# Optimization experiments

Measured on AMD Instinct MI355X. Metric: run time of the kernel, lower is better.

## Reference

```python
import jax, jax.numpy as jnp
import numpy as np

MAX_ANTS = 16  # padded max draws per (batch, neuron); ragged draws masked with -1
BS, N_IN, N_OUT = 32, 4096, 4096


def setup_inputs() -> dict:
    key = jax.random.key(0)
    k1, k2 = jax.random.split(key)
    # integer ant counts per (batch, input neuron), in [0, MAX_ANTS)
    x = jax.random.randint(k1, (BS, N_IN), 0, MAX_ANTS, dtype=jnp.int32)
    # positive weights (original init is uniform 1/n_outputs; random positive is general)
    weights = jax.random.uniform(k2, (N_IN, N_OUT), dtype=jnp.float32, minval=0.01, maxval=1.0)
    return {"x": x, "weights": weights}


def reference(x, weights):
    """Vectorized equivalent of ACOLayer.forward.

    Original: for each batch b and input neuron i with count c = x[b, i] > 0,
    draw c iid categorical samples from row-normalized weights[i].
    Here: inverse-CDF sampling, padded to MAX_ANTS draws, invalid slots = -1.
    Returns int32 [bs, n_in, MAX_ANTS].
    """
    probs = weights / weights.sum(axis=1, keepdims=True)   # normalize()
    cdf = jnp.cumsum(probs, axis=1)                        # [n_in, n_out]
    bs, n_in = x.shape
    n_out = weights.shape[1]
    u = jax.random.uniform(jax.random.key(42), (bs, n_in, MAX_ANTS), dtype=weights.dtype)
    # group draws by input neuron so each row's CDF is searched once
    u_rows = u.transpose(1, 0, 2).reshape(n_in, bs * MAX_ANTS)  # [n_in, bs*MAX]
    idx = jax.vmap(jnp.searchsorted)(cdf, u_rows)               # inverse-CDF draw
    idx = jnp.minimum(idx, n_out - 1).astype(jnp.int32)
    idx = idx.reshape(n_in, bs, MAX_ANTS).transpose(1, 0, 2)    # [bs, n_in, MAX]
    valid = jnp.arange(MAX_ANTS, dtype=x.dtype)[None, None, :] < x[:, :, None]
    return jnp.where(valid, idx, -1)
```

## Files before the change

### kernel.cpp

```cpp
#include <hip/hip_runtime.h>
#include <stdint.h>


#define N_IN    4096
#define N_OUT   4096
#define BS      32
#define MAX_A   16
#define THREADS 256
#define HALF    1048576u

__device__ __forceinline__ int padi(int j) { return j + (j >> 5); }

__device__ __forceinline__ uint32_t rotl32(uint32_t x, uint32_t r) {
    return (x << r) | (x >> (32u - r));
}

__device__ __forceinline__ void threefry2x32_42(uint32_t x0, uint32_t x1,
                                                uint32_t& o0, uint32_t& o1) {
    const uint32_t k0 = 0u, k1 = 42u;
    const uint32_t k2 = k0 ^ k1 ^ 0x1BD11BDAu;
    x0 += k0; x1 += k1;
#define TF_R(r) { x0 += x1; x1 = rotl32(x1, (r)); x1 ^= x0; }
    TF_R(13) TF_R(15) TF_R(26) TF_R(6)
    x0 += k1; x1 += k2 + 1u;
    TF_R(17) TF_R(29) TF_R(16) TF_R(24)
    x0 += k2; x1 += k0 + 2u;
    TF_R(13) TF_R(15) TF_R(26) TF_R(6)
    x0 += k0; x1 += k1 + 3u;
    TF_R(17) TF_R(29) TF_R(16) TF_R(24)
    x0 += k1; x1 += k2 + 4u;
    TF_R(13) TF_R(15) TF_R(26) TF_R(6)
    x0 += k2; x1 += k0 + 5u;
#undef TF_R
    o0 = x0; o1 = x1;
}

__device__ __forceinline__ float bits_to_uniform(uint32_t b) {
    uint32_t f = (b >> 9) | 0x3f800000u;
    float r;
    __builtin_memcpy(&r, &f, 4);
    return r - 1.0f;
}

__device__ __forceinline__ int tree4(float t,
    float T1, float T2, float T3, float T4, float T5, float T6, float T7,
    float T8, float T9, float T10, float T11, float T12, float T13,
    float T14, float T15) {
    const bool c1 = (T8 < t);
    const float m2 = c1 ? T12 : T4;
    const bool c2 = (m2 < t);
    const float ma = c2 ? T6  : T2;
    const float mb = c2 ? T14 : T10;
    const float m3 = c1 ? mb : ma;
    const bool c3 = (m3 < t);
    const float a1 = c3 ? T3  : T1;
    const float a2 = c3 ? T7  : T5;
    const float a3 = c3 ? T11 : T9;
    const float a4 = c3 ? T15 : T13;
    const float b1 = c2 ? a2 : a1;
    const float b2 = c2 ? a4 : a3;
    const float m4 = c1 ? b2 : b1;
    const bool c4 = (m4 < t);
    return (c1 ? 8 : 0) | (c2 ? 4 : 0) | (c3 ? 2 : 0) | (c4 ? 1 : 0);
}

__global__ __launch_bounds__(THREADS)
void aco_sample_kernel(const int* __restrict__ x,
                       const float* __restrict__ w,
                       int* __restrict__ out) {
    __shared__ float cdf[N_OUT + (N_OUT >> 5)];
    __shared__ float wsum[4];
    __shared__ int   xc[BS];

    const int row  = blockIdx.x;
    const int t    = threadIdx.x;
    const int lane = t & 63;
    const int wid  = t >> 6;

    const float4* wrow = (const float4*)(w + (size_t)row * N_OUT);
    float4 v0 = wrow[t * 4 + 0];
    float4 v1 = wrow[t * 4 + 1];
    float4 v2 = wrow[t * 4 + 2];
    float4 v3 = wrow[t * 4 + 3];

    if (t < BS) xc[t] = x[t * N_IN + row];

    const int bb = t >> 4;
    const int aa = t & 15;
    const uint32_t j0 = (uint32_t)(bb * (N_IN * MAX_A) + row * MAX_A + aa);
    const uint32_t j1 = j0 + HALF;
    uint32_t o0, o1, p0, p1;
    threefry2x32_42(0u, j0, o0, o1);
    threefry2x32_42(0u, j1, p0, p1);
    const float u0 = bits_to_uniform(o0 ^ o1);
    const float u1 = bits_to_uniform(p0 ^ p1);

    float loc[16];
    {
        float s = 0.f;
        s += v0.x; loc[0]  = s;  s += v0.y; loc[1]  = s;
        s += v0.z; loc[2]  = s;  s += v0.w; loc[3]  = s;
        s += v1.x; loc[4]  = s;  s += v1.y; loc[5]  = s;
        s += v1.z; loc[6]  = s;  s += v1.w; loc[7]  = s;
        s += v2.x; loc[8]  = s;  s += v2.y; loc[9]  = s;
        s += v2.z; loc[10] = s;  s += v2.w; loc[11] = s;
        s += v3.x; loc[12] = s;  s += v3.y; loc[13] = s;
        s += v3.z; loc[14] = s;  s += v3.w; loc[15] = s;
    }
    const float my_total = loc[15];

    float incl = my_total;
    #pragma unroll
    for (int d = 1; d < 64; d <<= 1) {
        float n = __shfl_up(incl, d, 64);
        if (lane >= d) incl += n;
    }
    if (lane == 63) wsum[wid] = incl;
    __syncthreads();

    const float4 ws = *(const float4*)wsum;
    const float total = ws.x + ws.y + ws.z + ws.w;
    float wprefix = 0.f;
    if (wid > 0) wprefix += ws.x;
    if (wid > 1) wprefix += ws.y;
    if (wid > 2) wprefix += ws.z;
    const float chunk_prefix = wprefix + incl - my_total;

    {
        const int base = t * 16;
        #pragma unroll
        for (int m = 0; m < 16; ++m)
            cdf[padi(base + m)] = chunk_prefix + loc[m];
    }
    __syncthreads();

    const float T1  = cdf[padi( 1 << 8)];
    const float T2  = cdf[padi( 2 << 8)];
    const float T3  = cdf[padi( 3 << 8)];
    const float T4  = cdf[padi( 4 << 8)];
    const float T5  = cdf[padi( 5 << 8)];
    const float T6  = cdf[padi( 6 << 8)];
    const float T7  = cdf[padi( 7 << 8)];
    const float T8  = cdf[padi( 8 << 8)];
    const float T9  = cdf[padi( 9 << 8)];
    const float T10 = cdf[padi(10 << 8)];
    const float T11 = cdf[padi(11 << 8)];
    const float T12 = cdf[padi(12 << 8)];
    const float T13 = cdf[padi(13 << 8)];
    const float T14 = cdf[padi(14 << 8)];
    const float T15 = cdf[padi(15 << 8)];

    const float t0 = u0 * total;
    const float t1 = u1 * total;

    const int ja = tree4(t0, T1,T2,T3,T4,T5,T6,T7,T8,T9,T10,T11,T12,T13,T14,T15);
    const int jb = tree4(t1, T1,T2,T3,T4,T5,T6,T7,T8,T9,T10,T11,T12,T13,T14,T15);
    int lo0 = ja << 8, hi0 = lo0 + 256;
    int lo1 = jb << 8, hi1 = lo1 + 256;
    #pragma unroll
    for (int it = 0; it < 8; ++it) {
        const int m0 = (lo0 + hi0) >> 1;
        const int m1 = (lo1 + hi1) >> 1;
        const float f0 = cdf[padi(m0)];
        const float f1 = cdf[padi(m1)];
        if (f0 < t0) lo0 = m0 + 1; else hi0 = m0;
        if (f1 < t1) lo1 = m1 + 1; else hi1 = m1;
    }
    const int idx0 = lo0 < N_OUT ? lo0 : N_OUT - 1;
    const int idx1 = lo1 < N_OUT ? lo1 : N_OUT - 1;

    out[j0] = (aa < xc[bb])      ? idx0 : -1;
    out[j1] = (aa < xc[bb + 16]) ? idx1 : -1;
}

extern "C" void kernel_launch(void* const* d_in, const int* in_sizes, int n_in,
                              void* d_out, int out_size, void* d_ws, size_t ws_size,
                              hipStream_t stream) {
    const int*   x;
    const float* w;
    if (in_sizes[0] == BS * N_IN) { x = (const int*)d_in[0]; w = (const float*)d_in[1]; }
    else                          { x = (const int*)d_in[1]; w = (const float*)d_in[0]; }
    aco_sample_kernel<<<N_IN, THREADS, 0, stream>>>(x, w, (int*)d_out);
}
```

Baseline: 20.92 us.

## Coalesce weight row loads with strided float4 chunks and four parallel scans

Each thread now loads four float4s spaced 256 apart, so consecutive lanes read consecutive 16-byte words and the global loads coalesce fully. Before, each thread read 64 contiguous bytes. The scan is restructured into four independent wavefront scans, one per quarter of the row, combined through shared memory. This costs four times as many shuffles, and the shared-memory CDF write pattern changes, which may affect bank conflicts. Floating-point summation order also changes slightly.

```diff
diff --git a/kernel.cpp b/kernel.cpp
--- a/kernel.cpp
+++ b/kernel.cpp
@@ -68,20 +68,20 @@
 void aco_sample_kernel(const int* __restrict__ x,
                        const float* __restrict__ w,
                        int* __restrict__ out) {
-    __shared__ float cdf[N_OUT + (N_OUT >> 5)];
-    __shared__ float wsum[4];
-    __shared__ int   xc[BS];
+    __shared__ float  cdf[N_OUT + (N_OUT >> 5)];
+    __shared__ float4 wsum4[4];
+    __shared__ int    xc[BS];
 
     const int row  = blockIdx.x;
     const int t    = threadIdx.x;
     const int lane = t & 63;
     const int wid  = t >> 6;
 
-    const float4* wrow = (const float4*)(w + (size_t)row * N_OUT);
-    float4 v0 = wrow[t * 4 + 0];
-    float4 v1 = wrow[t * 4 + 1];
-    float4 v2 = wrow[t * 4 + 2];
-    float4 v3 = wrow[t * 4 + 3];
+    const float4* wrow4 = (const float4*)(w + (size_t)row * N_OUT);
+    float4 v0 = wrow4[t];
+    float4 v1 = wrow4[t + 256];
+    float4 v2 = wrow4[t + 512];
+    float4 v3 = wrow4[t + 768];
 
     if (t < BS) xc[t] = x[t * N_IN + row];
 
@@ -95,42 +95,58 @@
     const float u0 = bits_to_uniform(o0 ^ o1);
     const float u1 = bits_to_uniform(p0 ^ p1);
 
-    float loc[16];
-    {
-        float s = 0.f;
-        s += v0.x; loc[0]  = s;  s += v0.y; loc[1]  = s;
-        s += v0.z; loc[2]  = s;  s += v0.w; loc[3]  = s;
-        s += v1.x; loc[4]  = s;  s += v1.y; loc[5]  = s;
-        s += v1.z; loc[6]  = s;  s += v1.w; loc[7]  = s;
-        s += v2.x; loc[8]  = s;  s += v2.y; loc[9]  = s;
-        s += v2.z; loc[10] = s;  s += v2.w; loc[11] = s;
-        s += v3.x; loc[12] = s;  s += v3.y; loc[13] = s;
-        s += v3.z; loc[14] = s;  s += v3.w; loc[15] = s;
-    }
-    const float my_total = loc[15];
-
-    float incl = my_total;
+    float4 s;
+    s.x = v0.x + v0.y + v0.z + v0.w;
+    s.y = v1.x + v1.y + v1.z + v1.w;
+    s.z = v2.x + v2.y + v2.z + v2.w;
+    s.w = v3.x + v3.y + v3.z + v3.w;
+
+    float4 incl = s;
     #pragma unroll
     for (int d = 1; d < 64; d <<= 1) {
-        float n = __shfl_up(incl, d, 64);
-        if (lane >= d) incl += n;
+        float nx = __shfl_up(incl.x, d, 64);
+        float ny = __shfl_up(incl.y, d, 64);
+        float nz = __shfl_up(incl.z, d, 64);
+        float nw = __shfl_up(incl.w, d, 64);
+        if (lane >= d) { incl.x += nx; incl.y += ny; incl.z += nz; incl.w += nw; }
     }
-    if (lane == 63) wsum[wid] = incl;
+    if (lane == 63) wsum4[wid] = incl;
     __syncthreads();
 
-    const float4 ws = *(const float4*)wsum;
-    const float total = ws.x + ws.y + ws.z + ws.w;
-    float wprefix = 0.f;
-    if (wid > 0) wprefix += ws.x;
-    if (wid > 1) wprefix += ws.y;
-    if (wid > 2) wprefix += ws.z;
-    const float chunk_prefix = wprefix + incl - my_total;
+    const float4 W0 = wsum4[0], W1 = wsum4[1], W2 = wsum4[2], W3 = wsum4[3];
+    const float T0s = W0.x + W1.x + W2.x + W3.x;
+    const float T1s = W0.y + W1.y + W2.y + W3.y;
+    const float T2s = W0.z + W1.z + W2.z + W3.z;
+    const float T3s = W0.w + W1.w + W2.w + W3.w;
+    const float total = T0s + T1s + T2s + T3s;
+    float4 wp = make_float4(0.f, 0.f, 0.f, 0.f);
+    if (wid > 0) { wp.x += W0.x; wp.y += W0.y; wp.z += W0.z; wp.w += W0.w; }
+    if (wid > 1) { wp.x += W1.x; wp.y += W1.y; wp.z += W1.z; wp.w += W1.w; }
+    if (wid > 2) { wp.x += W2.x; wp.y += W2.y; wp.z += W2.z; wp.w += W2.w; }
+    const float E0 = 0.f               + wp.x + (incl.x - s.x);
+    const float E1 = T0s               + wp.y + (incl.y - s.y);
+    const float E2 = T0s + T1s         + wp.z + (incl.z - s.z);
+    const float E3 = T0s + T1s + T2s   + wp.w + (incl.w - s.w);
 
     {
-        const int base = t * 16;
-        #pragma unroll
-        for (int m = 0; m < 16; ++m)
-            cdf[padi(base + m)] = chunk_prefix + loc[m];
+        const int base = 4 * t;
+        float r;
+        r = E0 + v0.x; cdf[padi(base + 0)] = r;
+        r += v0.y;     cdf[padi(base + 1)] = r;
+        r += v0.z;     cdf[padi(base + 2)] = r;
+        r += v0.w;     cdf[padi(base + 3)] = r;
+        r = E1 + v1.x; cdf[padi(1024 + base + 0)] = r;
+        r += v1.y;     cdf[padi(1024 + base + 1)] = r;
+        r += v1.z;     cdf[padi(1024 + base + 2)] = r;
+        r += v1.w;     cdf[padi(1024 + base + 3)] = r;
+        r = E2 + v2.x; cdf[padi(2048 + base + 0)] = r;
+        r += v2.y;     cdf[padi(2048 + base + 1)] = r;
+        r += v2.z;     cdf[padi(2048 + base + 2)] = r;
+        r += v2.w;     cdf[padi(2048 + base + 3)] = r;
+        r = E3 + v3.x; cdf[padi(3072 + base + 0)] = r;
+        r += v3.y;     cdf[padi(3072 + base + 1)] = r;
+        r += v3.z;     cdf[padi(3072 + base + 2)] = r;
+        r += v3.w;     cdf[padi(3072 + base + 3)] = r;
     }
     __syncthreads();
 
```

Result: slower. 23.17 us (+10.8%).
